# Optimization experiments

Hardware: AMD Instinct MI355X
Metric: run time of the kernel (lower is better)

Reference implementation:

```python
import math
import jax, jax.numpy as jnp
import numpy as np

SAMPLE_RATE = 16000
N_BANDS = 3
_F_DARK = jnp.array([270.0, 800.0, 2300.0], dtype=jnp.float32)
_F_NEUTRAL = jnp.array([500.0, 1500.0, 2500.0], dtype=jnp.float32)
_F_BRIGHT = jnp.array([730.0, 2100.0, 3000.0], dtype=jnp.float32)
_Q_DARK = jnp.array([5.0, 5.0, 5.0], dtype=jnp.float32)
_Q_NEUTRAL = jnp.array([8.0, 8.0, 8.0], dtype=jnp.float32)
_Q_BRIGHT = jnp.array([12.0, 12.0, 12.0], dtype=jnp.float32)


def _interpolate_formants(level):
    # level: [B] in [0,1] -> freqs, qs: [B, n_bands]
    t_low = jnp.clip(level * 2.0, 0.0, 1.0)[:, None]
    t_high = jnp.clip((level - 0.5) * 2.0, 0.0, 1.0)[:, None]
    use_high = (level >= 0.5)[:, None]
    freqs_lo = (1.0 - t_low) * _F_DARK + t_low * _F_NEUTRAL
    qs_lo = (1.0 - t_low) * _Q_DARK + t_low * _Q_NEUTRAL
    freqs_hi = (1.0 - t_high) * _F_NEUTRAL + t_high * _F_BRIGHT
    qs_hi = (1.0 - t_high) * _Q_NEUTRAL + t_high * _Q_BRIGHT
    freqs = jnp.where(use_high, freqs_hi, freqs_lo)
    qs = jnp.where(use_high, qs_hi, qs_lo)
    return freqs, qs


def _biquad_bandpass_coeffs(freq_hz, q):
    # freq_hz, q: [B, n_bands] -> coeffs each [B, n_bands]; b1 is 0
    omega = (2.0 * math.pi / SAMPLE_RATE) * freq_hz
    sin_o = jnp.sin(omega)
    cos_o = jnp.cos(omega)
    alpha = sin_o / (2.0 * jnp.maximum(q, 0.5))
    a0 = 1.0 + alpha
    b0 = alpha / a0
    b2 = -alpha / a0
    a1 = (-2.0 * cos_o) / a0
    a2 = (1.0 - alpha) / a0
    return b0, b2, a1, a2


def setup_inputs() -> dict:
    key = jax.random.key(0)
    k1, k2 = jax.random.split(key)
    B, S = 256, 131072
    audio = jax.random.normal(k1, (B, S), dtype=jnp.float32)
    resonance_level = jax.random.uniform(k2, (B,), dtype=jnp.float32)
    return {"audio": audio, "resonance_level": resonance_level}


def reference(audio, resonance_level):
    B, S = audio.shape
    level = jnp.clip(resonance_level.astype(audio.dtype), 0.0, 1.0)
    freqs, qs = _interpolate_formants(level)          # [B, nb]
    b0, b2, a1, a2 = _biquad_bandpass_coeffs(freqs, qs)
    # broadcast coeffs to [nb, B] for the scan
    b0, b2, a1, a2 = (c.T for c in (b0, b2, a1, a2))
    nb = N_BANDS
    zeros = jnp.zeros((nb, B), dtype=audio.dtype)
    inv_sqrt_nb = 1.0 / math.sqrt(nb)

    def step(carry, x_t):
        # carry: (x1, x2, y1, y2) each [nb, B]; x_t: [B]
        x1, x2, y1, y2 = carry
        y = b0 * x_t[None, :] + b2 * x2 - a1 * y1 - a2 * y2  # [nb, B]
        new_x1 = jnp.broadcast_to(x_t[None, :], (nb, B))
        return (new_x1, x1, y, y1), jnp.sum(y, axis=0) * inv_sqrt_nb

    _, out = jax.lax.scan(step, (zeros, zeros, zeros, zeros), audio.T)  # out: [S, B]
    return out.T
```

## Files before the change

kernel.cpp:

```cpp
#include <hip/hip_runtime.h>
#include <math.h>

#ifndef M_PI
#define M_PI 3.14159265358979323846
#endif

#define BATCHES 256
#define S_LEN   131072

#define TPB   256
#define CCH   32
#define SEGS  16
#define SEG_SAMPS (TPB * CCH)
#define WCH   24
#define NCH   (TPB + WCH)
#define OBSTR 33
#define SCAN_OFF 8448
#define SCAN_STR 281
#define H_OFF 10136
#define LDSF  10232

typedef float v4f __attribute__((ext_vector_type(4)));

__device__ __forceinline__ void compute_coeffs(float level_in, float b0[3], float na1[3], float na2[3]) {
    const float FD[3] = {270.0f, 800.0f, 2300.0f};
    const float FN[3] = {500.0f, 1500.0f, 2500.0f};
    const float FB[3] = {730.0f, 2100.0f, 3000.0f};
    float level = fminf(fmaxf(level_in, 0.0f), 1.0f);
    float t_low  = fminf(fmaxf(level * 2.0f, 0.0f), 1.0f);
    float t_high = fminf(fmaxf((level - 0.5f) * 2.0f, 0.0f), 1.0f);
    bool hi = (level >= 0.5f);
    const float W0 = (float)(2.0 * M_PI / 16000.0);
    #pragma unroll
    for (int k = 0; k < 3; ++k) {
        float f, q;
        if (hi) { f = (1.0f - t_high) * FN[k] + t_high * FB[k];
                  q = (1.0f - t_high) * 8.0f  + t_high * 12.0f; }
        else    { f = (1.0f - t_low) * FD[k] + t_low * FN[k];
                  q = (1.0f - t_low) * 5.0f  + t_low * 8.0f; }
        float omega = W0 * f;
        float sn = sinf(omega), cs = cosf(omega);
        float alpha = sn / (2.0f * fmaxf(q, 0.5f));
        float a0 = 1.0f + alpha;
        b0[k]  = alpha / a0;
        na1[k] = (2.0f * cs) / a0;
        na2[k] = -((1.0f - alpha) / a0);
    }
}

#define STEP3(XT, XTM2, SUMV)                                                    \
    {                                                                            \
        float d = (XT) - (XTM2);                                                 \
        float e0 = fmaf(b0[0], d, na2[0] * y2[0]);                               \
        float e1 = fmaf(b0[1], d, na2[1] * y2[1]);                               \
        float e2 = fmaf(b0[2], d, na2[2] * y2[2]);                               \
        float yy0 = fmaf(na1[0], y1[0], e0);                                     \
        float yy1 = fmaf(na1[1], y1[1], e1);                                     \
        float yy2 = fmaf(na1[2], y1[2], e2);                                     \
        y2[0] = y1[0]; y1[0] = yy0;                                              \
        y2[1] = y1[1]; y1[1] = yy1;                                              \
        y2[2] = y1[2]; y1[2] = yy2;                                              \
        SUMV = (yy0 + yy1 + yy2);                                                \
    }

#define MMUL(R00,R01,R10,R11, X00,X01,X10,X11, Y00,Y01,Y10,Y11)                  \
    {                                                                            \
        R00 = X00*Y00 + X01*Y10; R01 = X00*Y01 + X01*Y11;                        \
        R10 = X10*Y00 + X11*Y10; R11 = X10*Y01 + X11*Y11;                        \
    }

__global__ __launch_bounds__(TPB, 4)
void formant_onepass(const float* __restrict__ x, const float* __restrict__ lvl,
                     float* __restrict__ out)
{
    __shared__ float lds[LDSF];

    const int tid = threadIdx.x;
    const int row = blockIdx.x >> 4;
    const int seg = blockIdx.x & (SEGS - 1);

    float b0[3], na1[3], na2[3];
    compute_coeffs(lvl[row], b0, na1, na2);

    const float* xrow = x + (size_t)row * S_LEN;
    const size_t segBase = (size_t)seg * SEG_SAMPS;
    const float* xc = xrow + segBase + (size_t)tid * CCH;

    {
        float xm1 = 0.f, xm2 = 0.f;
        if (seg > 0 || tid > 0) { float2 t2 = *(const float2*)(xc - 2); xm2 = t2.x; xm1 = t2.y; }
        float y1[3] = {0.f,0.f,0.f}, y2[3] = {0.f,0.f,0.f};
        const float4* xv = (const float4*)xc;
        float* myob = lds + tid * OBSTR;
        float4 buf[4];
        #pragma unroll
        for (int j = 0; j < 4; ++j) buf[j] = xv[j];
        #pragma unroll
        for (int i = 0; i < 8; ++i) {
            float4 q = buf[i & 3];
            if (i + 4 < 8) buf[i & 3] = xv[i + 4];
            float4 o;
            STEP3(q.x, xm2, o.x)
            STEP3(q.y, xm1, o.y)
            STEP3(q.z, q.x, o.z)
            STEP3(q.w, q.y, o.w)
            xm2 = q.z; xm1 = q.w;
            myob[4*i + 0] = o.x;
            myob[4*i + 1] = o.y;
            myob[4*i + 2] = o.z;
            myob[4*i + 3] = o.w;
        }
        lds[SCAN_OFF + 0*SCAN_STR + WCH + tid] = y1[0];
        lds[SCAN_OFF + 1*SCAN_STR + WCH + tid] = y2[0];
        lds[SCAN_OFF + 2*SCAN_STR + WCH + tid] = y1[1];
        lds[SCAN_OFF + 3*SCAN_STR + WCH + tid] = y2[1];
        lds[SCAN_OFF + 4*SCAN_STR + WCH + tid] = y1[2];
        lds[SCAN_OFF + 5*SCAN_STR + WCH + tid] = y2[2];
    }

    if (tid < WCH) {
        if (seg == 0) {
            #pragma unroll
            for (int e = 0; e < 6; ++e) lds[SCAN_OFF + e*SCAN_STR + tid] = 0.f;
        } else {
            const float* xw = xrow + segBase - (size_t)(WCH * CCH) + (size_t)tid * CCH;
            float2 t2 = *(const float2*)(xw - 2);
            float y1[3] = {0.f,0.f,0.f}, y2[3] = {0.f,0.f,0.f};
            float p2 = t2.x, p1 = t2.y, dummy;
            const float4* xv = (const float4*)xw;
            float4 buf[4];
            #pragma unroll
            for (int j = 0; j < 4; ++j) buf[j] = xv[j];
            #pragma unroll
            for (int i = 0; i < 8; ++i) {
                float4 q = buf[i & 3];
                if (i + 4 < 8) buf[i & 3] = xv[i + 4];
                STEP3(q.x, p2, dummy)
                STEP3(q.y, p1, dummy)
                STEP3(q.z, q.x, dummy)
                STEP3(q.w, q.y, dummy)
                p2 = q.z; p1 = q.w;
            }
            (void)dummy;
            lds[SCAN_OFF + 0*SCAN_STR + tid] = y1[0];
            lds[SCAN_OFF + 1*SCAN_STR + tid] = y2[0];
            lds[SCAN_OFF + 2*SCAN_STR + tid] = y1[1];
            lds[SCAN_OFF + 3*SCAN_STR + tid] = y2[1];
            lds[SCAN_OFF + 4*SCAN_STR + tid] = y1[2];
            lds[SCAN_OFF + 5*SCAN_STR + tid] = y2[2];
        }
    }
    __syncthreads();

    {
        const int wv = tid >> 6, ln = tid & 63;
        if (wv < 3) {
            const float A1 = na1[wv], A2 = na2[wv];
            float hm1 = 1.f, hm2 = 0.f, hm3 = 0.f;
            for (int i = 0; i < CCH; ++i) {
                float h = fmaf(A1, hm1, A2 * hm2);
                hm3 = hm2; hm2 = hm1; hm1 = h;
                if (ln == 0) lds[H_OFF + wv * CCH + i] = h;
            }
            const float H00 = hm1, H01 = A2 * hm2;
            const float H10 = hm2, H11 = A2 * hm3;

            float* z1p = lds + SCAN_OFF + (2*wv) * SCAN_STR;
            float* z2p = lds + SCAN_OFF + (2*wv + 1) * SCAN_STR;

            const int cnt = (ln < 24) ? 5 : 4;
            const int beg = (ln < 24) ? 5 * ln : 120 + 4 * (ln - 24);

            float s1 = 0.f, s2 = 0.f;
            for (int j = 0; j < cnt; ++j) {
                float z1 = z1p[beg + j], z2 = z2p[beg + j];
                float n1 = z1 + H00 * s1 + H01 * s2;
                float n2 = z2 + H10 * s1 + H11 * s2;
                s1 = n1; s2 = n2;
            }
            float B00,B01,B10,B11, C00,C01,C10,C11;
            MMUL(B00,B01,B10,B11, H00,H01,H10,H11, H00,H01,H10,H11)
            MMUL(C00,C01,C10,C11, B00,B01,B10,B11, B00,B01,B10,B11)
            float A00 = C00, A01 = C01, A10 = C10, A11 = C11;
            if (cnt == 5) {
                float D00,D01,D10,D11;
                MMUL(D00,D01,D10,D11, C00,C01,C10,C11, H00,H01,H10,H11)
                A00 = D00; A01 = D01; A10 = D10; A11 = D11;
            }
            float bb1 = s1, bb2 = s2;
            for (int d = 1; d < 64; d <<= 1) {
                float iA00 = __shfl_up(A00, d), iA01 = __shfl_up(A01, d);
                float iA10 = __shfl_up(A10, d), iA11 = __shfl_up(A11, d);
                float ib1  = __shfl_up(bb1, d), ib2  = __shfl_up(bb2, d);
                if (ln >= d) {
                    float nb1 = A00 * ib1 + A01 * ib2 + bb1;
                    float nb2 = A10 * ib1 + A11 * ib2 + bb2;
                    float n00, n01, n10, n11;
                    MMUL(n00,n01,n10,n11, A00,A01,A10,A11, iA00,iA01,iA10,iA11)
                    A00 = n00; A01 = n01; A10 = n10; A11 = n11;
                    bb1 = nb1; bb2 = nb2;
                }
            }
            float e1 = __shfl_up(bb1, 1), e2 = __shfl_up(bb2, 1);
            if (ln == 0) { e1 = 0.f; e2 = 0.f; }

            s1 = e1; s2 = e2;
            for (int j = 0; j < cnt; ++j) {
                int w = beg + j;
                float z1 = z1p[w], z2 = z2p[w];
                z1p[w] = s1; z2p[w] = s2;
                float n1 = z1 + H00 * s1 + H01 * s2;
                float n2 = z2 + H10 * s1 + H11 * s2;
                s1 = n1; s2 = n2;
            }
        }
    }
    __syncthreads();

    {
        const float is3 = 0.57735026918962576f;
        float* obase = out + (size_t)row * S_LEN + segBase;
        #pragma unroll
        for (int j = 0; j < 8; ++j) {
            const int f   = j * TPB + tid;
            const int ch  = f >> 3;
            const int off = f & 7;
            const int t   = off * 4;
            const float* sp = lds + ch * OBSTR + t;
            float o0 = sp[0], o1 = sp[1], o2 = sp[2], o3 = sp[3];
            #pragma unroll
            for (int k = 0; k < 3; ++k) {
                const float c1 = lds[SCAN_OFF + (2*k)   * SCAN_STR + WCH + ch];
                const float c2 = na2[k] * lds[SCAN_OFF + (2*k+1) * SCAN_STR + WCH + ch];
                const float4 hv = *(const float4*)&lds[H_OFF + k * CCH + t];
                const float hm = (off == 0) ? 1.0f : lds[H_OFF + k * CCH + t - 1];
                o0 = fmaf(c1, hv.x, fmaf(c2, hm,   o0));
                o1 = fmaf(c1, hv.y, fmaf(c2, hv.x, o1));
                o2 = fmaf(c1, hv.z, fmaf(c2, hv.y, o2));
                o3 = fmaf(c1, hv.w, fmaf(c2, hv.z, o3));
            }
            v4f o = { o0 * is3, o1 * is3, o2 * is3, o3 * is3 };
            __builtin_nontemporal_store(o, (v4f*)(obase + (size_t)f * 4));
        }
    }
}

extern "C" void kernel_launch(void* const* d_in, const int* in_sizes, int n_in,
                              void* d_out, int out_size, void* d_ws, size_t ws_size,
                              hipStream_t stream) {
    const float* audio = (const float*)d_in[0];
    const float* level = (const float*)d_in[1];
    float* out = (float*)d_out;
    (void)in_sizes; (void)n_in; (void)d_ws; (void)ws_size; (void)out_size;

    formant_onepass<<<BATCHES * SEGS, TPB, 0, stream>>>(audio, level, out);
}
```

Before: 57.54 us.

## Run warm-up chunks on a dedicated fifth wavefront instead of serializing

Grows the block from 256 to 320 threads so the 24 warm-up chunk computations run on a separate wavefront, concurrently with the 256 main-chunk threads, rather than being done afterwards by the first 24 threads. The output stage is redistributed across 320 threads with a partial final iteration. Coefficient sin/cos also switch to fast intrinsics. The larger block with launch bounds of 4 blocks per CU raises register pressure and may reduce occupancy, and the fast trig intrinsics slightly change coefficient accuracy.

```diff
diff --git a/kernel.cpp b/kernel.cpp
--- a/kernel.cpp
+++ b/kernel.cpp
@@ -8,12 +8,12 @@
 #define BATCHES 256
 #define S_LEN   131072
 
-#define TPB   256
+#define TPB   320
+#define MAINT 256
 #define CCH   32
 #define SEGS  16
-#define SEG_SAMPS (TPB * CCH)
+#define SEG_SAMPS (MAINT * CCH)
 #define WCH   24
-#define NCH   (TPB + WCH)
 #define OBSTR 33
 #define SCAN_OFF 8448
 #define SCAN_STR 281
@@ -39,7 +39,7 @@
         else    { f = (1.0f - t_low) * FD[k] + t_low * FN[k];
                   q = (1.0f - t_low) * 5.0f  + t_low * 8.0f; }
         float omega = W0 * f;
-        float sn = sinf(omega), cs = cosf(omega);
+        float sn = __sinf(omega), cs = __cosf(omega);
         float alpha = sn / (2.0f * fmaxf(q, 0.5f));
         float a0 = 1.0f + alpha;
         b0[k]  = alpha / a0;
@@ -84,9 +84,9 @@
 
     const float* xrow = x + (size_t)row * S_LEN;
     const size_t segBase = (size_t)seg * SEG_SAMPS;
-    const float* xc = xrow + segBase + (size_t)tid * CCH;
-
-    {
+
+    if (tid < MAINT) {
+        const float* xc = xrow + segBase + (size_t)tid * CCH;
         float xm1 = 0.f, xm2 = 0.f;
         if (seg > 0 || tid > 0) { float2 t2 = *(const float2*)(xc - 2); xm2 = t2.x; xm1 = t2.y; }
         float y1[3] = {0.f,0.f,0.f}, y2[3] = {0.f,0.f,0.f};
@@ -117,13 +117,13 @@
         lds[SCAN_OFF + 4*SCAN_STR + WCH + tid] = y1[2];
         lds[SCAN_OFF + 5*SCAN_STR + WCH + tid] = y2[2];
     }
-
-    if (tid < WCH) {
+    else if (tid < MAINT + WCH) {
+        const int wid = tid - MAINT;
         if (seg == 0) {
             #pragma unroll
-            for (int e = 0; e < 6; ++e) lds[SCAN_OFF + e*SCAN_STR + tid] = 0.f;
+            for (int e = 0; e < 6; ++e) lds[SCAN_OFF + e*SCAN_STR + wid] = 0.f;
         } else {
-            const float* xw = xrow + segBase - (size_t)(WCH * CCH) + (size_t)tid * CCH;
+            const float* xw = xrow + segBase - (size_t)(WCH * CCH) + (size_t)wid * CCH;
             float2 t2 = *(const float2*)(xw - 2);
             float y1[3] = {0.f,0.f,0.f}, y2[3] = {0.f,0.f,0.f};
             float p2 = t2.x, p1 = t2.y, dummy;
@@ -142,12 +142,12 @@
                 p2 = q.z; p1 = q.w;
             }
             (void)dummy;
-            lds[SCAN_OFF + 0*SCAN_STR + tid] = y1[0];
-            lds[SCAN_OFF + 1*SCAN_STR + tid] = y2[0];
-            lds[SCAN_OFF + 2*SCAN_STR + tid] = y1[1];
-            lds[SCAN_OFF + 3*SCAN_STR + tid] = y2[1];
-            lds[SCAN_OFF + 4*SCAN_STR + tid] = y1[2];
-            lds[SCAN_OFF + 5*SCAN_STR + tid] = y2[2];
+            lds[SCAN_OFF + 0*SCAN_STR + wid] = y1[0];
+            lds[SCAN_OFF + 1*SCAN_STR + wid] = y2[0];
+            lds[SCAN_OFF + 2*SCAN_STR + wid] = y1[1];
+            lds[SCAN_OFF + 3*SCAN_STR + wid] = y2[1];
+            lds[SCAN_OFF + 4*SCAN_STR + wid] = y1[2];
+            lds[SCAN_OFF + 5*SCAN_STR + wid] = y2[2];
         }
     }
     __syncthreads();
@@ -220,28 +220,37 @@
     {
         const float is3 = 0.57735026918962576f;
         float* obase = out + (size_t)row * S_LEN + segBase;
+
+#define EMIT_OUT(F)                                                              \
+        {                                                                        \
+            const int f   = (F);                                                 \
+            const int ch  = f >> 3;                                              \
+            const int off = f & 7;                                               \
+            const int t   = off * 4;                                             \
+            const float* sp = lds + ch * OBSTR + t;                              \
+            float o0 = sp[0], o1 = sp[1], o2 = sp[2], o3 = sp[3];                \
+            _Pragma("unroll")                                                    \
+            for (int k = 0; k < 3; ++k) {                                        \
+                const float c1 = lds[SCAN_OFF + (2*k)   * SCAN_STR + WCH + ch];  \
+                const float c2 = na2[k] *                                        \
+                    lds[SCAN_OFF + (2*k+1) * SCAN_STR + WCH + ch];               \
+                const float4 hv = *(const float4*)&lds[H_OFF + k * CCH + t];     \
+                const float hm = (off == 0) ? 1.0f : lds[H_OFF + k*CCH + t - 1]; \
+                o0 = fmaf(c1, hv.x, fmaf(c2, hm,   o0));                         \
+                o1 = fmaf(c1, hv.y, fmaf(c2, hv.x, o1));                         \
+                o2 = fmaf(c1, hv.z, fmaf(c2, hv.y, o2));                         \
+                o3 = fmaf(c1, hv.w, fmaf(c2, hv.z, o3));                         \
+            }                                                                    \
+            v4f o = { o0 * is3, o1 * is3, o2 * is3, o3 * is3 };                  \
+            __builtin_nontemporal_store(o, (v4f*)(obase + (size_t)f * 4));       \
+        }
+
         #pragma unroll
-        for (int j = 0; j < 8; ++j) {
-            const int f   = j * TPB + tid;
-            const int ch  = f >> 3;
-            const int off = f & 7;
-            const int t   = off * 4;
-            const float* sp = lds + ch * OBSTR + t;
-            float o0 = sp[0], o1 = sp[1], o2 = sp[2], o3 = sp[3];
-            #pragma unroll
-            for (int k = 0; k < 3; ++k) {
-                const float c1 = lds[SCAN_OFF + (2*k)   * SCAN_STR + WCH + ch];
-                const float c2 = na2[k] * lds[SCAN_OFF + (2*k+1) * SCAN_STR + WCH + ch];
-                const float4 hv = *(const float4*)&lds[H_OFF + k * CCH + t];
-                const float hm = (off == 0) ? 1.0f : lds[H_OFF + k * CCH + t - 1];
-                o0 = fmaf(c1, hv.x, fmaf(c2, hm,   o0));
-                o1 = fmaf(c1, hv.y, fmaf(c2, hv.x, o1));
-                o2 = fmaf(c1, hv.z, fmaf(c2, hv.y, o2));
-                o3 = fmaf(c1, hv.w, fmaf(c2, hv.z, o3));
-            }
-            v4f o = { o0 * is3, o1 * is3, o2 * is3, o3 * is3 };
-            __builtin_nontemporal_store(o, (v4f*)(obase + (size_t)f * 4));
-        }
+        for (int j = 0; j < 6; ++j)
+            EMIT_OUT(j * TPB + tid)
+        if (tid < 2048 - 6 * TPB)
+            EMIT_OUT(6 * TPB + tid)
+#undef EMIT_OUT
     }
 }
 
```

New measurement: 57.20 us. About the same (-0.6%).
